# Optimization experiments

Measured on AMD Instinct MI355X. Metric: run time of the kernel, lower is better.

The kernel has to match this reference:

```python
import jax, jax.numpy as jnp
import numpy as np

N, DIM = 4096, 1024

def setup_inputs() -> dict:
    key = jax.random.key(0)
    ks = jax.random.split(key, 5)
    scale = 1.0 / np.sqrt(DIM)
    return {
        "x": jax.random.normal(ks[0], (N, DIM), dtype=jnp.float32),
        "Wq": jax.random.normal(ks[1], (DIM, DIM), dtype=jnp.float32) * scale,
        "bq": jax.random.normal(ks[2], (DIM,), dtype=jnp.float32) * 0.01,
        "Wk": jax.random.normal(ks[3], (DIM, DIM), dtype=jnp.float32) * scale,
        "bk": jax.random.normal(ks[4], (DIM,), dtype=jnp.float32) * 0.01,
    }

def reference(x, Wq, bq, Wk, bk):
    # torch nn.Linear: y = x @ W.T + b
    q = x @ Wq.T + bq            # [N, D]
    k = x @ Wk.T + bk            # [N, D]
    scores = q @ k.T             # [N, N] (no 1/sqrt(d) scaling, as in source)
    attn = jax.nn.softmax(scores, axis=-1)
    return attn @ x              # weighted pooling over raw x (no value proj)
```

## Files before the change

kernel.cpp:

```cpp
#include <hip/hip_runtime.h>
#include <hip/hip_bf16.h>
#include <hip/hip_fp16.h>
#include <stdint.h>


using half8   = __attribute__((ext_vector_type(8))) _Float16;
using float4v = __attribute__((ext_vector_type(4))) float;
using int4v   = __attribute__((ext_vector_type(4))) int;
using uint2v  = __attribute__((ext_vector_type(2))) unsigned int;

#define QS        (6.0f / 32768.0f)
#define INV_S     (32768.0f / 6.0f)
#define INV_S256  (128.0f / 6.0f)
#define C_HH      (65536.0f * QS * QS)
#define C_X       (256.0f * QS * QS)

#define SX        (6.0f / 32768.0f)
#define SW        (0.25f / 32768.0f)
#define P_HH      (65536.0f * SX * SW)
#define P_X       (256.0f * SX * SW)

#define GLOAD_LDS16(gptr, ldsptr)                                              \
  __builtin_amdgcn_global_load_lds(                                            \
      (__attribute__((address_space(1))) void*)(uintptr_t)(gptr),              \
      (__attribute__((address_space(3))) void*)(unsigned)(uintptr_t)(ldsptr),  \
      16, 0, 0)

__device__ __forceinline__ void barrier_raw() {
  asm volatile("" ::: "memory");
  __builtin_amdgcn_s_barrier();
  asm volatile("" ::: "memory");
}

__device__ __forceinline__ int swz3(int row) {
  return (((row >> 2) & 3) << 1) ^ (row & 3);
}

__global__ __launch_bounds__(256, 2) void gemm_s_stats(
    const int8_t* __restrict__ Ahi, const int8_t* __restrict__ Alo,
    const int8_t* __restrict__ Bhi, const int8_t* __restrict__ Blo,
    _Float16* __restrict__ E, float2* __restrict__ stats)
{
  __shared__ __align__(16) int8_t smem[65536];
  int8_t* sAh = smem;
  int8_t* sAl = smem + 16384;
  int8_t* sBh = smem + 32768;
  int8_t* sBl = smem + 49152;

  const int tid  = threadIdx.x;
  const int wave = tid >> 6;
  const int lane = tid & 63;
  const int quad = lane >> 4;
  const int t16  = lane & 15;
  const int wm   = wave & 1;
  const int wn   = wave >> 1;
  const int row0 = blockIdx.y * 128;
  const int col0 = blockIdx.x * 128;

  const int seg  = lane & 3;
  const int rsub = lane >> 2;

  const int offA0 = (row0 + wave * 16 + rsub) * 2048 + seg * 16;
  const int offA1 = offA0 + 64 * 2048;
  const int offB0 = (col0 + wave * 16 + rsub) * 2048 + seg * 16;
  const int offB1 = offB0 + 64 * 2048;
  const int ldsT0 = (wave * 16) * 64;
  const int ldsT1 = (64 + wave * 16) * 64;

  int4v hh[4][4], cc[4][4];
#pragma unroll
  for (int i = 0; i < 4; ++i)
#pragma unroll
    for (int j = 0; j < 4; ++j) {
      hh[i][j] = (int4v){0, 0, 0, 0};
      cc[i][j] = (int4v){0, 0, 0, 0};
    }

  auto stage_k = [&](int ks, int b) {
    const int k0 = ks * 64;
    GLOAD_LDS16(Ahi + offA0 + k0, sAh + b * 8192 + ldsT0);
    GLOAD_LDS16(Ahi + offA1 + k0, sAh + b * 8192 + ldsT1);
    GLOAD_LDS16(Alo + offA0 + k0, sAl + b * 8192 + ldsT0);
    GLOAD_LDS16(Alo + offA1 + k0, sAl + b * 8192 + ldsT1);
    GLOAD_LDS16(Bhi + offB0 + k0, sBh + b * 8192 + ldsT0);
    GLOAD_LDS16(Bhi + offB1 + k0, sBh + b * 8192 + ldsT1);
    GLOAD_LDS16(Blo + offB0 + k0, sBl + b * 8192 + ldsT0);
    GLOAD_LDS16(Blo + offB1 + k0, sBl + b * 8192 + ldsT1);
  };

  stage_k(0, 0);
  asm volatile("s_waitcnt vmcnt(0)" ::: "memory");
  barrier_raw();

  int buf = 0;
  for (int ks = 0; ks < 16; ++ks) {
    if (ks < 15) stage_k(ks + 1, buf ^ 1);

    int4v ah[4], al[4], bh[4], bl[4];
#pragma unroll
    for (int i = 0; i < 4; ++i) {
      const int ao = buf * 8192 + (wm * 64 + i * 16 + t16) * 64 + quad * 16;
      ah[i] = *(const int4v*)(sAh + ao);
      al[i] = *(const int4v*)(sAl + ao);
    }
#pragma unroll
    for (int j = 0; j < 4; ++j) {
      const int bo = buf * 8192 + (wn * 64 + j * 16 + t16) * 64 + quad * 16;
      bh[j] = *(const int4v*)(sBh + bo);
      bl[j] = *(const int4v*)(sBl + bo);
    }

    __builtin_amdgcn_s_setprio(1);
#pragma unroll
    for (int i = 0; i < 4; ++i)
#pragma unroll
      for (int j = 0; j < 4; ++j) {
        hh[i][j] = __builtin_amdgcn_mfma_i32_16x16x64_i8(ah[i], bh[j], hh[i][j], 0, 0, 0);
        cc[i][j] = __builtin_amdgcn_mfma_i32_16x16x64_i8(ah[i], bl[j], cc[i][j], 0, 0, 0);
        cc[i][j] = __builtin_amdgcn_mfma_i32_16x16x64_i8(al[i], bh[j], cc[i][j], 0, 0, 0);
      }
    __builtin_amdgcn_s_setprio(0);

    if (ks < 15) asm volatile("s_waitcnt vmcnt(0)" ::: "memory");
    barrier_raw();
    buf ^= 1;
  }

  float* red = (float*)smem;

  float vv[4][4][4];
  float rmax[4][4];
#pragma unroll
  for (int i = 0; i < 4; ++i)
#pragma unroll
    for (int r = 0; r < 4; ++r) {
      float mx = -3.0e38f;
#pragma unroll
      for (int j = 0; j < 4; ++j) {
        float v = C_HH * (float)hh[i][j][r] + C_X * (float)cc[i][j][r];
        vv[i][j][r] = v;
        mx = fmaxf(mx, v);
      }
      mx = fmaxf(mx, __shfl_xor(mx, 1));
      mx = fmaxf(mx, __shfl_xor(mx, 2));
      mx = fmaxf(mx, __shfl_xor(mx, 4));
      mx = fmaxf(mx, __shfl_xor(mx, 8));
      rmax[i][r] = mx;
    }
  if (t16 == 0) {
#pragma unroll
    for (int i = 0; i < 4; ++i)
#pragma unroll
      for (int r = 0; r < 4; ++r)
        red[wn * 128 + wm * 64 + i * 16 + quad * 4 + r] = rmax[i][r];
  }
  __syncthreads();

  float mrow[4][4];
#pragma unroll
  for (int i = 0; i < 4; ++i)
#pragma unroll
    for (int r = 0; r < 4; ++r) {
      const int row = wm * 64 + i * 16 + quad * 4 + r;
      mrow[i][r] = fmaxf(red[row], red[128 + row]);
    }

  float rsum[4][4];
#pragma unroll
  for (int i = 0; i < 4; ++i)
#pragma unroll
    for (int r = 0; r < 4; ++r) {
      float s = 0.f;
#pragma unroll
      for (int j = 0; j < 4; ++j) {
        float e = __expf(vv[i][j][r] - mrow[i][r]);
        vv[i][j][r] = e;
        s += e;
      }
      s += __shfl_xor(s, 1);
      s += __shfl_xor(s, 2);
      s += __shfl_xor(s, 4);
      s += __shfl_xor(s, 8);
      rsum[i][r] = s;
    }
  if (t16 == 0) {
#pragma unroll
    for (int i = 0; i < 4; ++i)
#pragma unroll
      for (int r = 0; r < 4; ++r)
        red[256 + wn * 128 + wm * 64 + i * 16 + quad * 4 + r] = rsum[i][r];
  }

  uint16_t* img = (uint16_t*)(smem + 32768);
#pragma unroll
  for (int i = 0; i < 4; ++i)
#pragma unroll
    for (int j = 0; j < 4; ++j)
#pragma unroll
      for (int r = 0; r < 4; ++r) {
        const int row  = wm * 64 + i * 16 + quad * 4 + r;
        const int col  = wn * 64 + j * 16 + t16;
        const int colS = col ^ (((quad << 1) ^ r) << 3);
        _Float16 h = (_Float16)vv[i][j][r];
        img[row * 128 + colS] = *(const uint16_t*)&h;
      }
  __syncthreads();

#pragma unroll
  for (int it = 0; it < 8; ++it) {
    const int row    = wave * 32 + it * 4 + quad;
    const int chunkS = t16 ^ swz3(row);
    int4v v = *(const int4v*)&img[row * 128 + chunkS * 8];
    *(int4v*)&E[(size_t)(row0 + row) * 4096 + col0 + t16 * 8] = v;
  }

  if (wn == 0 && t16 == 0) {
#pragma unroll
    for (int i = 0; i < 4; ++i)
#pragma unroll
      for (int r = 0; r < 4; ++r) {
        const int row = wm * 64 + i * 16 + quad * 4 + r;
        const float l = red[256 + row] + red[256 + 128 + row];
        stats[(size_t)(row0 + row) * 32 + blockIdx.x] =
            make_float2(mrow[i][r], l);
      }
  }
}

__global__ __launch_bounds__(256, 2) void gemm_proj_i8(
    const int8_t* __restrict__ Ahi, const int8_t* __restrict__ Alo,
    const int8_t* __restrict__ Bhi, const int8_t* __restrict__ Blo,
    const float* __restrict__ biasQ, const float* __restrict__ biasK,
    int8_t* __restrict__ Ch, int8_t* __restrict__ Cl)
{
  __shared__ __align__(16) int8_t smem[65536];
  int8_t* sAh = smem;
  int8_t* sAl = smem + 16384;
  int8_t* sBh = smem + 32768;
  int8_t* sBl = smem + 49152;

  const int tid  = threadIdx.x;
  const int wave = tid >> 6;
  const int lane = tid & 63;
  const int quad = lane >> 4;
  const int t16  = lane & 15;
  const int wm   = wave & 1;
  const int wn   = wave >> 1;
  const int row0 = blockIdx.y * 128;
  const int col0 = blockIdx.x * 128;

  const int seg  = lane & 3;
  const int rsub = lane >> 2;

  const int offA0 = (row0 + wave * 16 + rsub) * 1024 + seg * 16;
  const int offA1 = offA0 + 64 * 1024;
  const int offB0 = (col0 + wave * 16 + rsub) * 1024 + seg * 16;
  const int offB1 = offB0 + 64 * 1024;
  const int ldsT0 = (wave * 16) * 64;
  const int ldsT1 = (64 + wave * 16) * 64;

  int4v hh[4][4], cc[4][4];
#pragma unroll
  for (int i = 0; i < 4; ++i)
#pragma unroll
    for (int j = 0; j < 4; ++j) {
      hh[i][j] = (int4v){0, 0, 0, 0};
      cc[i][j] = (int4v){0, 0, 0, 0};
    }

  auto stage_k = [&](int ks, int b) {
    const int k0 = ks * 64;
    GLOAD_LDS16(Ahi + offA0 + k0, sAh + b * 8192 + ldsT0);
    GLOAD_LDS16(Ahi + offA1 + k0, sAh + b * 8192 + ldsT1);
    GLOAD_LDS16(Alo + offA0 + k0, sAl + b * 8192 + ldsT0);
    GLOAD_LDS16(Alo + offA1 + k0, sAl + b * 8192 + ldsT1);
    GLOAD_LDS16(Bhi + offB0 + k0, sBh + b * 8192 + ldsT0);
    GLOAD_LDS16(Bhi + offB1 + k0, sBh + b * 8192 + ldsT1);
    GLOAD_LDS16(Blo + offB0 + k0, sBl + b * 8192 + ldsT0);
    GLOAD_LDS16(Blo + offB1 + k0, sBl + b * 8192 + ldsT1);
  };

  stage_k(0, 0);
  asm volatile("s_waitcnt vmcnt(0)" ::: "memory");
  barrier_raw();

  int buf = 0;
  for (int ks = 0; ks < 16; ++ks) {
    if (ks < 15) stage_k(ks + 1, buf ^ 1);

    int4v ah[4], al[4], bh[4], bl[4];
#pragma unroll
    for (int i = 0; i < 4; ++i) {
      const int ao = buf * 8192 + (wm * 64 + i * 16 + t16) * 64 + quad * 16;
      ah[i] = *(const int4v*)(sAh + ao);
      al[i] = *(const int4v*)(sAl + ao);
    }
#pragma unroll
    for (int j = 0; j < 4; ++j) {
      const int bo = buf * 8192 + (wn * 64 + j * 16 + t16) * 64 + quad * 16;
      bh[j] = *(const int4v*)(sBh + bo);
      bl[j] = *(const int4v*)(sBl + bo);
    }

    __builtin_amdgcn_s_setprio(1);
#pragma unroll
    for (int i = 0; i < 4; ++i)
#pragma unroll
      for (int j = 0; j < 4; ++j) {
        hh[i][j] = __builtin_amdgcn_mfma_i32_16x16x64_i8(ah[i], bh[j], hh[i][j], 0, 0, 0);
        cc[i][j] = __builtin_amdgcn_mfma_i32_16x16x64_i8(ah[i], bl[j], cc[i][j], 0, 0, 0);
        cc[i][j] = __builtin_amdgcn_mfma_i32_16x16x64_i8(al[i], bh[j], cc[i][j], 0, 0, 0);
      }
    __builtin_amdgcn_s_setprio(0);

    if (ks < 15) asm volatile("s_waitcnt vmcnt(0)" ::: "memory");
    barrier_raw();
    buf ^= 1;
  }

  uint16_t* img = (uint16_t*)(smem + 32768);
#pragma unroll
  for (int i = 0; i < 4; ++i) {
#pragma unroll
    for (int j = 0; j < 4; ++j) {
      const int ccol = col0 + wn * 64 + j * 16 + t16;
      const float* bp = (ccol < 1024) ? biasQ : (biasK - 1024);
#pragma unroll
      for (int r = 0; r < 4; ++r) {
        float v = P_HH * (float)hh[i][j][r] + P_X * (float)cc[i][j][r] + bp[ccol];
        int hi = (int)lrintf(v * INV_S256);
        hi = hi > 127 ? 127 : (hi < -127 ? -127 : hi);
        int lo = (int)lrintf(v * INV_S - 256.0f * (float)hi);
        lo = lo > 127 ? 127 : (lo < -127 ? -127 : lo);
        const int row  = wm * 64 + i * 16 + quad * 4 + r;
        const int col  = wn * 64 + j * 16 + t16;
        const int colS = col ^ (((quad << 1) ^ r) << 3);
        img[row * 128 + colS] = (uint16_t)((hi & 0xff) | ((lo & 0xff) << 8));
      }
    }
  }
  __syncthreads();

#pragma unroll
  for (int it = 0; it < 8; ++it) {
    const int row    = wave * 32 + it * 4 + quad;
    const int chunkS = t16 ^ swz3(row);
    int4v p = *(const int4v*)&img[row * 128 + chunkS * 8];
    const unsigned w0 = (unsigned)p[0], w1 = (unsigned)p[1];
    const unsigned w2 = (unsigned)p[2], w3 = (unsigned)p[3];
    uint2v hw, lw;
    hw[0] = (w0 & 0xffu) | (((w0 >> 16) & 0xffu) << 8) |
            ((w1 & 0xffu) << 16) | (((w1 >> 16) & 0xffu) << 24);
    hw[1] = (w2 & 0xffu) | (((w2 >> 16) & 0xffu) << 8) |
            ((w3 & 0xffu) << 16) | (((w3 >> 16) & 0xffu) << 24);
    lw[0] = ((w0 >> 8) & 0xffu) | (((w0 >> 24) & 0xffu) << 8) |
            (((w1 >> 8) & 0xffu) << 16) | ((w1 >> 24) << 24);
    lw[1] = ((w2 >> 8) & 0xffu) | (((w2 >> 24) & 0xffu) << 8) |
            (((w3 >> 8) & 0xffu) << 16) | ((w3 >> 24) << 24);
    const size_t go = (size_t)(row0 + row) * 2048 + col0 + t16 * 8;
    *(uint2v*)&Ch[go] = hw;
    *(uint2v*)&Cl[go] = lw;
  }
}

__global__ __launch_bounds__(512) void gemm_av(
    const uint16_t* __restrict__ E, const uint16_t* __restrict__ B,
    const float2* __restrict__ stats, float* __restrict__ out)
{
  __shared__ __align__(16) uint16_t stg[2][2][16384];
  __shared__ float betaS[128 * 33];

  const int L      = blockIdx.x;
  const int xcd    = L & 7;
  const int rest   = L >> 3;
  const int colb   = rest & 7;
  const int bandHi = rest >> 3;
  const int band   = xcd + 8 * bandHi;
  const int row0   = band * 128;
  const int col0   = colb * 128;

  const int tid  = threadIdx.x;
  const int wave = tid >> 6;
  const int z    = wave >> 2;
  const int gw   = wave & 3;
  const int lane = tid & 63;
  const int quad = lane >> 4;
  const int t16  = lane & 15;
  const int wm   = gw & 1;
  const int wn   = gw >> 1;

  const int c8   = lane & 7;
  const int r8   = lane >> 3;
  const int srcC = (c8 - r8) & 7;

  int offA[4], offB[4];
#pragma unroll
  for (int r = 0; r < 4; ++r) {
    offA[r] = (row0 + r * 32 + gw * 8 + r8) * 4096 + srcC * 8;
    offB[r] = (col0 + r * 32 + gw * 8 + r8) * 4096 + srcC * 8;
  }

  auto stage_s = [&](int s, int b) {
    const int k0h = (z * 16 + (s >> 1)) * 128 + (s & 1) * 64;
    uint16_t* sA = &stg[b][z][0];
    uint16_t* sB = &stg[b][z][8192];
#pragma unroll
    for (int r = 0; r < 4; ++r) {
      GLOAD_LDS16(E + offA[r] + k0h, &sA[(r * 32 + gw * 8) * 64]);
      GLOAD_LDS16(B + offB[r] + k0h, &sB[(r * 32 + gw * 8) * 64]);
    }
  };

  stage_s(0, 0);

  if (tid < 128) {
    const int row = row0 + tid;
    float2 st[32];
    float m = -3.0e38f;
#pragma unroll
    for (int t = 0; t < 32; ++t) {
      st[t] = stats[(size_t)row * 32 + t];
      m = fmaxf(m, st[t].x);
    }
    float l = 0.f;
#pragma unroll
    for (int t = 0; t < 32; ++t) l += st[t].y * __expf(st[t].x - m);
    const float inv = 1.0f / l;
#pragma unroll
    for (int t = 0; t < 32; ++t)
      betaS[tid * 33 + t] = __expf(st[t].x - m) * inv;
  }
  asm volatile("s_waitcnt vmcnt(0)" ::: "memory");
  __syncthreads();

  float4v acc[4][4];
#pragma unroll
  for (int i = 0; i < 4; ++i)
#pragma unroll
    for (int j = 0; j < 4; ++j)
      acc[i][j] = (float4v){0.f, 0.f, 0.f, 0.f};

  int buf = 0;
  for (int s = 0; s < 32; ++s) {
    if (s < 31) stage_s(s + 1, buf ^ 1);

    const int t = z * 16 + (s >> 1);
    _Float16 bb[4];
#pragma unroll
    for (int i = 0; i < 4; ++i)
      bb[i] = (_Float16)betaS[(wm * 64 + i * 16 + t16) * 33 + t];

    const uint16_t* sA = &stg[buf][z][0];
    const uint16_t* sB = &stg[buf][z][8192];

    half8 af[2][4], bf[2][4];
#pragma unroll
    for (int ks = 0; ks < 2; ++ks) {
#pragma unroll
      for (int i = 0; i < 4; ++i) {
        const int row = wm * 64 + i * 16 + t16;
        const int ch  = (ks * 4 + quad + (t16 & 7)) & 7;
        af[ks][i] = *(const half8*)&sA[row * 64 + ch * 8];
        half8 bs;
#pragma unroll
        for (int c = 0; c < 8; ++c) bs[c] = bb[i];
        af[ks][i] = af[ks][i] * bs;
      }
#pragma unroll
      for (int j = 0; j < 4; ++j) {
        const int row = wn * 64 + j * 16 + t16;
        const int ch  = (ks * 4 + quad + (t16 & 7)) & 7;
        bf[ks][j] = *(const half8*)&sB[row * 64 + ch * 8];
      }
    }

    __builtin_amdgcn_s_setprio(1);
#pragma unroll
    for (int ks = 0; ks < 2; ++ks)
#pragma unroll
      for (int i = 0; i < 4; ++i)
#pragma unroll
        for (int j = 0; j < 4; ++j)
          acc[i][j] = __builtin_amdgcn_mfma_f32_16x16x32_f16(af[ks][i], bf[ks][j], acc[i][j], 0, 0, 0);
    __builtin_amdgcn_s_setprio(0);

    if (s < 31) asm volatile("s_waitcnt vmcnt(0)" ::: "memory");
    barrier_raw();
    buf ^= 1;
  }

  float* xfer = (float*)stg;
#pragma unroll
  for (int h = 0; h < 2; ++h) {
    if (z == 1) {
#pragma unroll
      for (int i = 2 * h; i < 2 * h + 2; ++i)
#pragma unroll
        for (int j = 0; j < 4; ++j)
#pragma unroll
          for (int r = 0; r < 4; ++r) {
            const int e = (i - 2 * h) * 16 + j * 4 + r;
            xfer[e * 256 + gw * 64 + lane] = acc[i][j][r];
          }
    }
    __syncthreads();
    if (z == 0) {
#pragma unroll
      for (int i = 2 * h; i < 2 * h + 2; ++i)
#pragma unroll
        for (int j = 0; j < 4; ++j)
#pragma unroll
          for (int r = 0; r < 4; ++r) {
            const int e = (i - 2 * h) * 16 + j * 4 + r;
            acc[i][j][r] += xfer[e * 256 + gw * 64 + lane];
          }
    }
    __syncthreads();
  }

  float* img = (float*)((int8_t*)stg + 65536);
  if (z == 0) {
#pragma unroll
    for (int i = 0; i < 4; ++i)
#pragma unroll
      for (int j = 0; j < 4; ++j)
#pragma unroll
        for (int r = 0; r < 4; ++r) {
          const int row  = wm * 64 + i * 16 + quad * 4 + r;
          const int col  = wn * 64 + j * 16 + t16;
          const int colS = col ^ (((quad << 1) ^ r) << 2);
          img[row * 128 + colS] = acc[i][j][r];
        }
  }
  __syncthreads();

#pragma unroll
  for (int it = 0; it < 8; ++it) {
    const int row    = wave * 16 + (lane >> 2);
    const int chunk  = (lane & 3) * 8 + it;
    const int chunkS = chunk ^ swz3(row);
    float4v v = *(const float4v*)&img[row * 128 + chunkS * 4];
    *(float4v*)&out[(size_t)(row0 + row) * 1024 + col0 + chunk * 4] = v;
  }
}

__global__ __launch_bounds__(256) void quantT(
    const float* __restrict__ x, const float* __restrict__ Wq,
    const float* __restrict__ Wk,
    int8_t* __restrict__ xhi, int8_t* __restrict__ xlo,
    int8_t* __restrict__ whi, int8_t* __restrict__ wlo,
    uint16_t* __restrict__ xT)
{
  if (blockIdx.x < 6144) {
// ... 37 lines not shown
      const int oc = ty + p * 8;
      __half hv = __float2half_rn(tile[tx][oc]);
      xT[(size_t)(bx * 32 + oc) * 4096 + by * 32 + tx] = *(uint16_t*)&hv;
    }
  }
}

extern "C" void kernel_launch(void* const* d_in, const int* in_sizes, int n_in,
                              void* d_out, int out_size, void* d_ws, size_t ws_size,
                              hipStream_t stream) {
  const int N = 4096, D = 1024;
  const float* x  = (const float*)d_in[0];
  const float* Wq = (const float*)d_in[1];
  const float* bq = (const float*)d_in[2];
  const float* Wk = (const float*)d_in[3];
  const float* bk = (const float*)d_in[4];
  float* out = (float*)d_out;

  char* w = (char*)d_ws;
  const size_t MiB = 1024 * 1024;
  int8_t*    xq_hi  = (int8_t*)   (w + 0  * MiB);
  int8_t*    xq_lo  = (int8_t*)   (w + 4  * MiB);
  int8_t*    Wqk_hi = (int8_t*)   (w + 8  * MiB);
  int8_t*    Wqk_lo = (int8_t*)   (w + 10 * MiB);
  int8_t*    qk_hi  = (int8_t*)   (w + 12 * MiB);
  int8_t*    qk_lo  = (int8_t*)   (w + 20 * MiB);
  _Float16*  E      = (_Float16*) (w + 36 * MiB);
  float2*    stats  = (float2*)   (w + 68 * MiB);
  uint16_t*  xTh    = (uint16_t*) (w + 72 * MiB);

  quantT<<<10240, 256, 0, stream>>>(x, Wq, Wk, xq_hi, xq_lo, Wqk_hi, Wqk_lo,
                                    xTh);

  gemm_proj_i8<<<dim3(2048 / 128, N / 128), 256, 0, stream>>>(
      xq_hi, xq_lo, Wqk_hi, Wqk_lo, bq, bk, qk_hi, qk_lo);

  gemm_s_stats<<<dim3(N / 128, N / 128), 256, 0, stream>>>(
      qk_hi, qk_lo, qk_hi + 1024, qk_lo + 1024, E, stats);

  gemm_av<<<256, 512, 0, stream>>>((const uint16_t*)E, xTh, stats, out);

  (void)in_sizes; (void)n_in; (void)out_size; (void)ws_size;
}
```

Measured before the change: 218.2 us.

## Enlarge GEMM tiles to 256x128 with 512 threads and triple-buffer loads

The int8 projection and score GEMMs now use 256x128 tiles computed by 8 waves, which shares each B tile across more rows. Their shared-memory staging becomes a three-stage ring with partial vmcnt waits, so loads run two k-steps ahead of compute. The attention-times-x kernel also moves to three buffers with a smaller k chunk per stage. The aim is to hide global-load latency and cut B-operand traffic. In exchange each block needs 144KB of LDS, which drops residency to one block per CU and reduces the grid size.

```diff
diff --git a/kernel.cpp b/kernel.cpp
--- a/kernel.cpp
+++ b/kernel.cpp
@@ -36,36 +36,30 @@
   return (((row >> 2) & 3) << 1) ^ (row & 3);
 }
 
-__global__ __launch_bounds__(256, 2) void gemm_s_stats(
+__global__ __launch_bounds__(512, 2) void gemm_s_stats(
     const int8_t* __restrict__ Ahi, const int8_t* __restrict__ Alo,
     const int8_t* __restrict__ Bhi, const int8_t* __restrict__ Blo,
     _Float16* __restrict__ E, float2* __restrict__ stats)
 {
-  __shared__ __align__(16) int8_t smem[65536];
-  int8_t* sAh = smem;
-  int8_t* sAl = smem + 16384;
-  int8_t* sBh = smem + 32768;
-  int8_t* sBl = smem + 49152;
+  __shared__ __align__(16) int8_t smem[147456];
 
   const int tid  = threadIdx.x;
   const int wave = tid >> 6;
   const int lane = tid & 63;
   const int quad = lane >> 4;
   const int t16  = lane & 15;
-  const int wm   = wave & 1;
-  const int wn   = wave >> 1;
-  const int row0 = blockIdx.y * 128;
+  const int wm   = wave >> 1;
+  const int wn   = wave & 1;
+  const int row0 = blockIdx.y * 256;
   const int col0 = blockIdx.x * 128;
 
   const int seg  = lane & 3;
-  const int rsub = lane >> 2;
-
-  const int offA0 = (row0 + wave * 16 + rsub) * 2048 + seg * 16;
-  const int offA1 = offA0 + 64 * 2048;
-  const int offB0 = (col0 + wave * 16 + rsub) * 2048 + seg * 16;
-  const int offB1 = offB0 + 64 * 2048;
-  const int ldsT0 = (wave * 16) * 64;
-  const int ldsT1 = (64 + wave * 16) * 64;
+  const int arow = wave * 16 + (lane >> 2);
+
+  const int gA0 = (row0 + arow) * 2048 + seg * 16;
+  const int gA1 = gA0 + 128 * 2048;
+  const int gB0 = (col0 + arow) * 2048 + seg * 16;
+  const int ldsW = wave * 1024;
 
   int4v hh[4][4], cc[4][4];
 #pragma unroll
@@ -78,36 +72,36 @@
 
   auto stage_k = [&](int ks, int b) {
     const int k0 = ks * 64;
-    GLOAD_LDS16(Ahi + offA0 + k0, sAh + b * 8192 + ldsT0);
-    GLOAD_LDS16(Ahi + offA1 + k0, sAh + b * 8192 + ldsT1);
-    GLOAD_LDS16(Alo + offA0 + k0, sAl + b * 8192 + ldsT0);
-    GLOAD_LDS16(Alo + offA1 + k0, sAl + b * 8192 + ldsT1);
-    GLOAD_LDS16(Bhi + offB0 + k0, sBh + b * 8192 + ldsT0);
-    GLOAD_LDS16(Bhi + offB1 + k0, sBh + b * 8192 + ldsT1);
-    GLOAD_LDS16(Blo + offB0 + k0, sBl + b * 8192 + ldsT0);
-    GLOAD_LDS16(Blo + offB1 + k0, sBl + b * 8192 + ldsT1);
+    int8_t* base = smem + b * 49152;
+    GLOAD_LDS16(Ahi + gA0 + k0, base + ldsW);
+    GLOAD_LDS16(Ahi + gA1 + k0, base + 8192 + ldsW);
+    GLOAD_LDS16(Alo + gA0 + k0, base + 16384 + ldsW);
+    GLOAD_LDS16(Alo + gA1 + k0, base + 16384 + 8192 + ldsW);
+    GLOAD_LDS16(Bhi + gB0 + k0, base + 32768 + ldsW);
+    GLOAD_LDS16(Blo + gB0 + k0, base + 40960 + ldsW);
   };
 
   stage_k(0, 0);
-  asm volatile("s_waitcnt vmcnt(0)" ::: "memory");
+  stage_k(1, 1);
+  asm volatile("s_waitcnt vmcnt(6)" ::: "memory");
   barrier_raw();
 
-  int buf = 0;
   for (int ks = 0; ks < 16; ++ks) {
-    if (ks < 15) stage_k(ks + 1, buf ^ 1);
+    int8_t* base = smem + (ks % 3) * 49152;
+    if (ks < 14) stage_k(ks + 2, (ks + 2) % 3);
 
     int4v ah[4], al[4], bh[4], bl[4];
 #pragma unroll
     for (int i = 0; i < 4; ++i) {
-      const int ao = buf * 8192 + (wm * 64 + i * 16 + t16) * 64 + quad * 16;
-      ah[i] = *(const int4v*)(sAh + ao);
-      al[i] = *(const int4v*)(sAl + ao);
+      const int ao = (wm * 64 + i * 16 + t16) * 64 + quad * 16;
+      ah[i] = *(const int4v*)(base + ao);
+      al[i] = *(const int4v*)(base + 16384 + ao);
     }
 #pragma unroll
     for (int j = 0; j < 4; ++j) {
-      const int bo = buf * 8192 + (wn * 64 + j * 16 + t16) * 64 + quad * 16;
-      bh[j] = *(const int4v*)(sBh + bo);
-      bl[j] = *(const int4v*)(sBl + bo);
+      const int bo = (wn * 64 + j * 16 + t16) * 64 + quad * 16;
+      bh[j] = *(const int4v*)(base + 32768 + bo);
+      bl[j] = *(const int4v*)(base + 40960 + bo);
     }
 
     __builtin_amdgcn_s_setprio(1);
@@ -121,12 +115,15 @@
       }
     __builtin_amdgcn_s_setprio(0);
 
-    if (ks < 15) asm volatile("s_waitcnt vmcnt(0)" ::: "memory");
-    barrier_raw();
-    buf ^= 1;
-  }
-
-  float* red = (float*)smem;
+    if (ks < 15) {
+      if (ks < 14) asm volatile("s_waitcnt vmcnt(6)" ::: "memory");
+      else         asm volatile("s_waitcnt vmcnt(0)" ::: "memory");
+      barrier_raw();
+    }
+  }
+  barrier_raw();
+
+  float* red = (float*)(smem + 65536);
 
   float vv[4][4][4];
   float rmax[4][4];
@@ -152,7 +149,7 @@
     for (int i = 0; i < 4; ++i)
 #pragma unroll
       for (int r = 0; r < 4; ++r)
-        red[wn * 128 + wm * 64 + i * 16 + quad * 4 + r] = rmax[i][r];
+        red[wn * 256 + wm * 64 + i * 16 + quad * 4 + r] = rmax[i][r];
   }
   __syncthreads();
 
@@ -162,7 +159,7 @@
 #pragma unroll
     for (int r = 0; r < 4; ++r) {
       const int row = wm * 64 + i * 16 + quad * 4 + r;
-      mrow[i][r] = fmaxf(red[row], red[128 + row]);
+      mrow[i][r] = fmaxf(red[row], red[256 + row]);
     }
 
   float rsum[4][4];
@@ -188,10 +185,10 @@
     for (int i = 0; i < 4; ++i)
 #pragma unroll
       for (int r = 0; r < 4; ++r)
-        red[256 + wn * 128 + wm * 64 + i * 16 + quad * 4 + r] = rsum[i][r];
-  }
-
-  uint16_t* img = (uint16_t*)(smem + 32768);
+        red[512 + wn * 256 + wm * 64 + i * 16 + quad * 4 + r] = rsum[i][r];
+  }
+
+  uint16_t* img = (uint16_t*)smem;
 #pragma unroll
   for (int i = 0; i < 4; ++i)
 #pragma unroll
@@ -200,7 +197,7 @@
       for (int r = 0; r < 4; ++r) {
         const int row  = wm * 64 + i * 16 + quad * 4 + r;
         const int col  = wn * 64 + j * 16 + t16;
-        const int colS = col ^ (((quad << 1) ^ r) << 3);
+        const int colS = col ^ (swz3(row) << 3);
         _Float16 h = (_Float16)vv[i][j][r];
         img[row * 128 + colS] = *(const uint16_t*)&h;
       }
@@ -214,50 +211,38 @@
     *(int4v*)&E[(size_t)(row0 + row) * 4096 + col0 + t16 * 8] = v;
   }
 
-  if (wn == 0 && t16 == 0) {
-#pragma unroll
-    for (int i = 0; i < 4; ++i)
-#pragma unroll
-      for (int r = 0; r < 4; ++r) {
-        const int row = wm * 64 + i * 16 + quad * 4 + r;
-        const float l = red[256 + row] + red[256 + 128 + row];
-        stats[(size_t)(row0 + row) * 32 + blockIdx.x] =
-            make_float2(mrow[i][r], l);
-      }
+  if (tid < 256) {
+    const float m = fmaxf(red[tid], red[256 + tid]);
+    const float l = red[512 + tid] + red[768 + tid];
+    stats[(size_t)(row0 + tid) * 32 + blockIdx.x] = make_float2(m, l);
   }
 }
 
-__global__ __launch_bounds__(256, 2) void gemm_proj_i8(
+__global__ __launch_bounds__(512, 2) void gemm_proj_i8(
     const int8_t* __restrict__ Ahi, const int8_t* __restrict__ Alo,
     const int8_t* __restrict__ Bhi, const int8_t* __restrict__ Blo,
     const float* __restrict__ biasQ, const float* __restrict__ biasK,
     int8_t* __restrict__ Ch, int8_t* __restrict__ Cl)
 {
-  __shared__ __align__(16) int8_t smem[65536];
-  int8_t* sAh = smem;
-  int8_t* sAl = smem + 16384;
-  int8_t* sBh = smem + 32768;
-  int8_t* sBl = smem + 49152;
+  __shared__ __align__(16) int8_t smem[147456];
 
   const int tid  = threadIdx.x;
   const int wave = tid >> 6;
   const int lane = tid & 63;
   const int quad = lane >> 4;
   const int t16  = lane & 15;
-  const int wm   = wave & 1;
-  const int wn   = wave >> 1;
-  const int row0 = blockIdx.y * 128;
+  const int wm   = wave >> 1;
+  const int wn   = wave & 1;
+  const int row0 = blockIdx.y * 256;
   const int col0 = blockIdx.x * 128;
 
   const int seg  = lane & 3;
-  const int rsub = lane >> 2;
-
-  const int offA0 = (row0 + wave * 16 + rsub) * 1024 + seg * 16;
-  const int offA1 = offA0 + 64 * 1024;
-  const int offB0 = (col0 + wave * 16 + rsub) * 1024 + seg * 16;
-  const int offB1 = offB0 + 64 * 1024;
-  const int ldsT0 = (wave * 16) * 64;
-  const int ldsT1 = (64 + wave * 16) * 64;
+  const int arow = wave * 16 + (lane >> 2);
+
+  const int gA0 = (row0 + arow) * 1024 + seg * 16;
+  const int gA1 = gA0 + 128 * 1024;
+  const int gB0 = (col0 + arow) * 1024 + seg * 16;
+  const int ldsW = wave * 1024;
 
   int4v hh[4][4], cc[4][4];
 #pragma unroll
@@ -270,36 +255,36 @@
 
   auto stage_k = [&](int ks, int b) {
     const int k0 = ks * 64;
-    GLOAD_LDS16(Ahi + offA0 + k0, sAh + b * 8192 + ldsT0);
-    GLOAD_LDS16(Ahi + offA1 + k0, sAh + b * 8192 + ldsT1);
-    GLOAD_LDS16(Alo + offA0 + k0, sAl + b * 8192 + ldsT0);
-    GLOAD_LDS16(Alo + offA1 + k0, sAl + b * 8192 + ldsT1);
-    GLOAD_LDS16(Bhi + offB0 + k0, sBh + b * 8192 + ldsT0);
-    GLOAD_LDS16(Bhi + offB1 + k0, sBh + b * 8192 + ldsT1);
-    GLOAD_LDS16(Blo + offB0 + k0, sBl + b * 8192 + ldsT0);
-    GLOAD_LDS16(Blo + offB1 + k0, sBl + b * 8192 + ldsT1);
+    int8_t* base = smem + b * 49152;
+    GLOAD_LDS16(Ahi + gA0 + k0, base + ldsW);
+    GLOAD_LDS16(Ahi + gA1 + k0, base + 8192 + ldsW);
+    GLOAD_LDS16(Alo + gA0 + k0, base + 16384 + ldsW);
+    GLOAD_LDS16(Alo + gA1 + k0, base + 16384 + 8192 + ldsW);
+    GLOAD_LDS16(Bhi + gB0 + k0, base + 32768 + ldsW);
+    GLOAD_LDS16(Blo + gB0 + k0, base + 40960 + ldsW);
   };
 
   stage_k(0, 0);
-  asm volatile("s_waitcnt vmcnt(0)" ::: "memory");
+  stage_k(1, 1);
+  asm volatile("s_waitcnt vmcnt(6)" ::: "memory");
   barrier_raw();
 
-  int buf = 0;
   for (int ks = 0; ks < 16; ++ks) {
-    if (ks < 15) stage_k(ks + 1, buf ^ 1);
+    int8_t* base = smem + (ks % 3) * 49152;
+    if (ks < 14) stage_k(ks + 2, (ks + 2) % 3);
 
     int4v ah[4], al[4], bh[4], bl[4];
 #pragma unroll
     for (int i = 0; i < 4; ++i) {
-      const int ao = buf * 8192 + (wm * 64 + i * 16 + t16) * 64 + quad * 16;
-      ah[i] = *(const int4v*)(sAh + ao);
-      al[i] = *(const int4v*)(sAl + ao);
+      const int ao = (wm * 64 + i * 16 + t16) * 64 + quad * 16;
+      ah[i] = *(const int4v*)(base + ao);
+      al[i] = *(const int4v*)(base + 16384 + ao);
     }
 #pragma unroll
     for (int j = 0; j < 4; ++j) {
-      const int bo = buf * 8192 + (wn * 64 + j * 16 + t16) * 64 + quad * 16;
-      bh[j] = *(const int4v*)(sBh + bo);
-      bl[j] = *(const int4v*)(sBl + bo);
+      const int bo = (wn * 64 + j * 16 + t16) * 64 + quad * 16;
+      bh[j] = *(const int4v*)(base + 32768 + bo);
+      bl[j] = *(const int4v*)(base + 40960 + bo);
     }
 
     __builtin_amdgcn_s_setprio(1);
@@ -313,12 +298,15 @@
       }
     __builtin_amdgcn_s_setprio(0);
 
-    if (ks < 15) asm volatile("s_waitcnt vmcnt(0)" ::: "memory");
-    barrier_raw();
-    buf ^= 1;
-  }
-
-  uint16_t* img = (uint16_t*)(smem + 32768);
+    if (ks < 15) {
+      if (ks < 14) asm volatile("s_waitcnt vmcnt(6)" ::: "memory");
+      else         asm volatile("s_waitcnt vmcnt(0)" ::: "memory");
+      barrier_raw();
+    }
+  }
+  barrier_raw();
+
+  uint16_t* img = (uint16_t*)smem;
 #pragma unroll
   for (int i = 0; i < 4; ++i) {
 #pragma unroll
@@ -334,7 +322,7 @@
         lo = lo > 127 ? 127 : (lo < -127 ? -127 : lo);
         const int row  = wm * 64 + i * 16 + quad * 4 + r;
         const int col  = wn * 64 + j * 16 + t16;
-        const int colS = col ^ (((quad << 1) ^ r) << 3);
+        const int colS = col ^ (swz3(row) << 3);
         img[row * 128 + colS] = (uint16_t)((hi & 0xff) | ((lo & 0xff) << 8));
       }
     }
@@ -367,7 +355,7 @@
     const uint16_t* __restrict__ E, const uint16_t* __restrict__ B,
     const float2* __restrict__ stats, float* __restrict__ out)
 {
-  __shared__ __align__(16) uint16_t stg[2][2][16384];
+  __shared__ __align__(16) uint16_t stg[3][16384];
   __shared__ float betaS[128 * 33];
 
   const int L      = blockIdx.x;
@@ -389,29 +377,26 @@
   const int wm   = gw & 1;
   const int wn   = gw >> 1;
 
-  const int c8   = lane & 7;
-  const int r8   = lane >> 3;
-  const int srcC = (c8 - r8) & 7;
-
-  int offA[4], offB[4];
-#pragma unroll
-  for (int r = 0; r < 4; ++r) {
-    offA[r] = (row0 + r * 32 + gw * 8 + r8) * 4096 + srcC * 8;
-    offB[r] = (col0 + r * 32 + gw * 8 + r8) * 4096 + srcC * 8;
-  }
+  const int seg  = lane & 3;
+  const int grow = gw * 16 + (lane >> 2);
+
+  const int offA0 = (row0 + grow) * 4096 + seg * 8;
+  const int offA1 = offA0 + 64 * 4096;
+  const int offB0 = (col0 + grow) * 4096 + seg * 8;
+  const int offB1 = offB0 + 64 * 4096;
+  const int ldsW  = gw * 512;
 
   auto stage_s = [&](int s, int b) {
-    const int k0h = (z * 16 + (s >> 1)) * 128 + (s & 1) * 64;
-    uint16_t* sA = &stg[b][z][0];
-    uint16_t* sB = &stg[b][z][8192];
-#pragma unroll
-    for (int r = 0; r < 4; ++r) {
-      GLOAD_LDS16(E + offA[r] + k0h, &sA[(r * 32 + gw * 8) * 64]);
-      GLOAD_LDS16(B + offB[r] + k0h, &sB[(r * 32 + gw * 8) * 64]);
-    }
+    const int k0h = (z * 16 + (s >> 2)) * 128 + (s & 3) * 32;
+    uint16_t* dst = &stg[b][z * 8192];
+    GLOAD_LDS16(E + offA0 + k0h, dst + ldsW);
+    GLOAD_LDS16(E + offA1 + k0h, dst + 2048 + ldsW);
+    GLOAD_LDS16(B + offB0 + k0h, dst + 4096 + ldsW);
+    GLOAD_LDS16(B + offB1 + k0h, dst + 4096 + 2048 + ldsW);
   };
 
   stage_s(0, 0);
+  stage_s(1, 1);
 
   if (tid < 128) {
     const int row = row0 + tid;
@@ -430,7 +415,7 @@
     for (int t = 0; t < 32; ++t)
       betaS[tid * 33 + t] = __expf(st[t].x - m) * inv;
   }
-  asm volatile("s_waitcnt vmcnt(0)" ::: "memory");
+  asm volatile("s_waitcnt vmcnt(4)" ::: "memory");
   __syncthreads();
 
   float4v acc[4][4];
@@ -440,54 +425,44 @@
     for (int j = 0; j < 4; ++j)
       acc[i][j] = (float4v){0.f, 0.f, 0.f, 0.f};
 
-  int buf = 0;
-  for (int s = 0; s < 32; ++s) {
-    if (s < 31) stage_s(s + 1, buf ^ 1);
-
-    const int t = z * 16 + (s >> 1);
+  for (int s = 0; s < 64; ++s) {
+    const uint16_t* base = &stg[s % 3][z * 8192];
+    if (s < 62) stage_s(s + 2, (s + 2) % 3);
+
+    const int t = z * 16 + (s >> 2);
     _Float16 bb[4];
 #pragma unroll
     for (int i = 0; i < 4; ++i)
       bb[i] = (_Float16)betaS[(wm * 64 + i * 16 + t16) * 33 + t];
 
-    const uint16_t* sA = &stg[buf][z][0];
-    const uint16_t* sB = &stg[buf][z][8192];
-
-    half8 af[2][4], bf[2][4];
-#pragma unroll
-    for (int ks = 0; ks < 2; ++ks) {
-#pragma unroll
-      for (int i = 0; i < 4; ++i) {
-        const int row = wm * 64 + i * 16 + t16;
-        const int ch  = (ks * 4 + quad + (t16 & 7)) & 7;
-        af[ks][i] = *(const half8*)&sA[row * 64 + ch * 8];
-        half8 bs;
-#pragma unroll
-        for (int c = 0; c < 8; ++c) bs[c] = bb[i];
-        af[ks][i] = af[ks][i] * bs;
-      }
-#pragma unroll
-      for (int j = 0; j < 4; ++j) {
-        const int row = wn * 64 + j * 16 + t16;
-        const int ch  = (ks * 4 + quad + (t16 & 7)) & 7;
-        bf[ks][j] = *(const half8*)&sB[row * 64 + ch * 8];
-      }
-    }
+    half8 af[4], bf[4];
+#pragma unroll
+    for (int i = 0; i < 4; ++i) {
+      af[i] = *(const half8*)&base[(wm * 64 + i * 16 + t16) * 32 + quad * 8];
+      half8 bs;
+#pragma unroll
+      for (int c = 0; c < 8; ++c) bs[c] = bb[i];
+      af[i] = af[i] * bs;
+    }
+#pragma unroll
+    for (int j = 0; j < 4; ++j)
+      bf[j] = *(const half8*)&base[4096 + (wn * 64 + j * 16 + t16) * 32 + quad * 8];
 
     __builtin_amdgcn_s_setprio(1);
 #pragma unroll
-    for (int ks = 0; ks < 2; ++ks)
-#pragma unroll
-      for (int i = 0; i < 4; ++i)
-#pragma unroll
-        for (int j = 0; j < 4; ++j)
-          acc[i][j] = __builtin_amdgcn_mfma_f32_16x16x32_f16(af[ks][i], bf[ks][j], acc[i][j], 0, 0, 0);
+    for (int i = 0; i < 4; ++i)
+#pragma unroll
+      for (int j = 0; j < 4; ++j)
+        acc[i][j] = __builtin_amdgcn_mfma_f32_16x16x32_f16(af[i], bf[j], acc[i][j], 0, 0, 0);
     __builtin_amdgcn_s_setprio(0);
 
-    if (s < 31) asm volatile("s_waitcnt vmcnt(0)" ::: "memory");
-    barrier_raw();
-    buf ^= 1;
-  }
+    if (s < 63) {
+      if (s < 62) asm volatile("s_waitcnt vmcnt(4)" ::: "memory");
+      else        asm volatile("s_waitcnt vmcnt(0)" ::: "memory");
+      barrier_raw();
+    }
+  }
+  barrier_raw();
 
   float* xfer = (float*)stg;
 #pragma unroll
@@ -518,7 +493,7 @@
     __syncthreads();
   }
 
-  float* img = (float*)((int8_t*)stg + 65536);
+  float* img = (float*)stg;
   if (z == 0) {
 #pragma unroll
     for (int i = 0; i < 4; ++i)
@@ -622,10 +597,10 @@
   quantT<<<10240, 256, 0, stream>>>(x, Wq, Wk, xq_hi, xq_lo, Wqk_hi, Wqk_lo,
                                     xTh);
 
-  gemm_proj_i8<<<dim3(2048 / 128, N / 128), 256, 0, stream>>>(
+  gemm_proj_i8<<<dim3(2048 / 128, N / 256), 512, 0, stream>>>(
       xq_hi, xq_lo, Wqk_hi, Wqk_lo, bq, bk, qk_hi, qk_lo);
 
-  gemm_s_stats<<<dim3(N / 128, N / 128), 256, 0, stream>>>(
+  gemm_s_stats<<<dim3(N / 128, N / 256), 512, 0, stream>>>(
       qk_hi, qk_lo, qk_hi + 1024, qk_lo + 1024, E, stats);
 
   gemm_av<<<256, 512, 0, stream>>>((const uint16_t*)E, xTh, stats, out);
```

New measurement: 223.5 us. +2.4%, slower.

## Load E fragments directly to registers and halve LDS staging in gemm_av

Applied to the files above, without the earlier changes.

In gemm_av, the E (probability) operand is now read straight from global memory into register fragments, double-buffered across steps. Only B goes through LDS, which halves the LDS staging buffer and changes the B swizzle to XOR. This should lower LDS traffic and footprint, which may allow more occupancy. The trade-offs are more registers, uncoalesced-ish global reads for E, and the img region now aliasing the xfer area. The int8 GEMMs also reorder their LDS loads and MFMA issue into three separate passes, which may improve instruction interleaving.

```diff
diff --git a/kernel.cpp b/kernel.cpp
--- a/kernel.cpp
+++ b/kernel.cpp
@@ -101,12 +101,20 @@
     for (int i = 0; i < 4; ++i) {
       const int ao = buf * 8192 + (wm * 64 + i * 16 + t16) * 64 + quad * 16;
       ah[i] = *(const int4v*)(sAh + ao);
-      al[i] = *(const int4v*)(sAl + ao);
     }
 #pragma unroll
     for (int j = 0; j < 4; ++j) {
       const int bo = buf * 8192 + (wn * 64 + j * 16 + t16) * 64 + quad * 16;
       bh[j] = *(const int4v*)(sBh + bo);
+    }
+#pragma unroll
+    for (int i = 0; i < 4; ++i) {
+      const int ao = buf * 8192 + (wm * 64 + i * 16 + t16) * 64 + quad * 16;
+      al[i] = *(const int4v*)(sAl + ao);
+    }
+#pragma unroll
+    for (int j = 0; j < 4; ++j) {
+      const int bo = buf * 8192 + (wn * 64 + j * 16 + t16) * 64 + quad * 16;
       bl[j] = *(const int4v*)(sBl + bo);
     }
 
@@ -114,11 +122,18 @@
 #pragma unroll
     for (int i = 0; i < 4; ++i)
 #pragma unroll
-      for (int j = 0; j < 4; ++j) {
+      for (int j = 0; j < 4; ++j)
         hh[i][j] = __builtin_amdgcn_mfma_i32_16x16x64_i8(ah[i], bh[j], hh[i][j], 0, 0, 0);
+#pragma unroll
+    for (int i = 0; i < 4; ++i)
+#pragma unroll
+      for (int j = 0; j < 4; ++j)
         cc[i][j] = __builtin_amdgcn_mfma_i32_16x16x64_i8(ah[i], bl[j], cc[i][j], 0, 0, 0);
+#pragma unroll
+    for (int i = 0; i < 4; ++i)
+#pragma unroll
+      for (int j = 0; j < 4; ++j)
         cc[i][j] = __builtin_amdgcn_mfma_i32_16x16x64_i8(al[i], bh[j], cc[i][j], 0, 0, 0);
-      }
     __builtin_amdgcn_s_setprio(0);
 
     if (ks < 15) asm volatile("s_waitcnt vmcnt(0)" ::: "memory");
@@ -293,12 +308,20 @@
     for (int i = 0; i < 4; ++i) {
       const int ao = buf * 8192 + (wm * 64 + i * 16 + t16) * 64 + quad * 16;
       ah[i] = *(const int4v*)(sAh + ao);
-      al[i] = *(const int4v*)(sAl + ao);
     }
 #pragma unroll
     for (int j = 0; j < 4; ++j) {
       const int bo = buf * 8192 + (wn * 64 + j * 16 + t16) * 64 + quad * 16;
       bh[j] = *(const int4v*)(sBh + bo);
+    }
+#pragma unroll
+    for (int i = 0; i < 4; ++i) {
+      const int ao = buf * 8192 + (wm * 64 + i * 16 + t16) * 64 + quad * 16;
+      al[i] = *(const int4v*)(sAl + ao);
+    }
+#pragma unroll
+    for (int j = 0; j < 4; ++j) {
+      const int bo = buf * 8192 + (wn * 64 + j * 16 + t16) * 64 + quad * 16;
       bl[j] = *(const int4v*)(sBl + bo);
     }
 
@@ -306,11 +329,18 @@
 #pragma unroll
     for (int i = 0; i < 4; ++i)
 #pragma unroll
-      for (int j = 0; j < 4; ++j) {
+      for (int j = 0; j < 4; ++j)
         hh[i][j] = __builtin_amdgcn_mfma_i32_16x16x64_i8(ah[i], bh[j], hh[i][j], 0, 0, 0);
+#pragma unroll
+    for (int i = 0; i < 4; ++i)
+#pragma unroll
+      for (int j = 0; j < 4; ++j)
         cc[i][j] = __builtin_amdgcn_mfma_i32_16x16x64_i8(ah[i], bl[j], cc[i][j], 0, 0, 0);
+#pragma unroll
+    for (int i = 0; i < 4; ++i)
+#pragma unroll
+      for (int j = 0; j < 4; ++j)
         cc[i][j] = __builtin_amdgcn_mfma_i32_16x16x64_i8(al[i], bh[j], cc[i][j], 0, 0, 0);
-      }
     __builtin_amdgcn_s_setprio(0);
 
     if (ks < 15) asm volatile("s_waitcnt vmcnt(0)" ::: "memory");
@@ -367,7 +397,7 @@
     const uint16_t* __restrict__ E, const uint16_t* __restrict__ B,
     const float2* __restrict__ stats, float* __restrict__ out)
 {
-  __shared__ __align__(16) uint16_t stg[2][2][16384];
+  __shared__ __align__(16) uint16_t stg[2][2][8192];
   __shared__ float betaS[128 * 33];
 
   const int L      = blockIdx.x;
@@ -389,29 +419,42 @@
   const int wm   = gw & 1;
   const int wn   = gw >> 1;
 
-  const int c8   = lane & 7;
-  const int r8   = lane >> 3;
-  const int srcC = (c8 - r8) & 7;
-
-  int offA[4], offB[4];
-#pragma unroll
-  for (int r = 0; r < 4; ++r) {
-    offA[r] = (row0 + r * 32 + gw * 8 + r8) * 4096 + srcC * 8;
-    offB[r] = (col0 + r * 32 + gw * 8 + r8) * 4096 + srcC * 8;
-  }
-
-  auto stage_s = [&](int s, int b) {
-    const int k0h = (z * 16 + (s >> 1)) * 128 + (s & 1) * 64;
-    uint16_t* sA = &stg[b][z][0];
-    uint16_t* sB = &stg[b][z][8192];
-#pragma unroll
-    for (int r = 0; r < 4; ++r) {
-      GLOAD_LDS16(E + offA[r] + k0h, &sA[(r * 32 + gw * 8) * 64]);
-      GLOAD_LDS16(B + offB[r] + k0h, &sB[(r * 32 + gw * 8) * 64]);
-    }
+  const int r8 = lane >> 3;
+  const int c8 = lane & 7;
+
+  int offE[2][4];
+#pragma unroll
+  for (int ks = 0; ks < 2; ++ks)
+#pragma unroll
+    for (int i = 0; i < 4; ++i)
+      offE[ks][i] = (row0 + wm * 64 + i * 16 + t16) * 4096 + z * 2048 +
+                    ks * 32 + quad * 8;
+
+  int offB[4];
+#pragma unroll
+  for (int p = 0; p < 4; ++p)
+    offB[p] = (col0 + p * 32 + gw * 8 + r8) * 8192 + z * 4096 + ((c8 ^ r8) * 16);
+
+  auto stage_B = [&](int s, int b) {
+    const int k0b = s * 128;
+    int8_t* dst = (int8_t*)&stg[b][z][0];
+#pragma unroll
+    for (int p = 0; p < 4; ++p)
+      GLOAD_LDS16((const int8_t*)B + offB[p] + k0b, dst + (p * 32 + gw * 8) * 128);
   };
 
-  stage_s(0, 0);
+  half8 afA[2][4], afB[2][4];
+  auto load_E = [&](int s, half8 (&dstf)[2][4]) {
+    const int k0h = s * 64;
+#pragma unroll
+    for (int ks = 0; ks < 2; ++ks)
+#pragma unroll
+      for (int i = 0; i < 4; ++i)
+        dstf[ks][i] = *(const half8*)&E[offE[ks][i] + k0h];
+  };
+
+  stage_B(0, 0);
+  load_E(0, afA);
 
   if (tid < 128) {
     const int row = row0 + tid;
@@ -440,9 +483,11 @@
     for (int j = 0; j < 4; ++j)
       acc[i][j] = (float4v){0.f, 0.f, 0.f, 0.f};
 
-  int buf = 0;
-  for (int s = 0; s < 32; ++s) {
-    if (s < 31) stage_s(s + 1, buf ^ 1);
+  auto step = [&](int s, int b, half8 (&cur)[2][4], half8 (&nxt)[2][4]) {
+    if (s < 31) {
+      load_E(s + 1, nxt);
+      stage_B(s + 1, b ^ 1);
+    }
 
     const int t = z * 16 + (s >> 1);
     _Float16 bb[4];
@@ -450,43 +495,43 @@
     for (int i = 0; i < 4; ++i)
       bb[i] = (_Float16)betaS[(wm * 64 + i * 16 + t16) * 33 + t];
 
-    const uint16_t* sA = &stg[buf][z][0];
-    const uint16_t* sB = &stg[buf][z][8192];
-
-    half8 af[2][4], bf[2][4];
-#pragma unroll
-    for (int ks = 0; ks < 2; ++ks) {
-#pragma unroll
-      for (int i = 0; i < 4; ++i) {
-        const int row = wm * 64 + i * 16 + t16;
-        const int ch  = (ks * 4 + quad + (t16 & 7)) & 7;
-        af[ks][i] = *(const half8*)&sA[row * 64 + ch * 8];
-        half8 bs;
-#pragma unroll
-        for (int c = 0; c < 8; ++c) bs[c] = bb[i];
-        af[ks][i] = af[ks][i] * bs;
-      }
+    const uint16_t* sB = &stg[b][z][0];
+    half8 bf[2][4];
+#pragma unroll
+    for (int ks = 0; ks < 2; ++ks)
 #pragma unroll
       for (int j = 0; j < 4; ++j) {
         const int row = wn * 64 + j * 16 + t16;
-        const int ch  = (ks * 4 + quad + (t16 & 7)) & 7;
+        const int ch  = (ks * 4 + quad) ^ (t16 & 7);
         bf[ks][j] = *(const half8*)&sB[row * 64 + ch * 8];
       }
-    }
 
     __builtin_amdgcn_s_setprio(1);
 #pragma unroll
-    for (int ks = 0; ks < 2; ++ks)
+    for (int ks = 0; ks < 2; ++ks) {
+      half8 afs[4];
+#pragma unroll
+      for (int i = 0; i < 4; ++i) {
+        half8 bs;
+#pragma unroll
+        for (int c = 0; c < 8; ++c) bs[c] = bb[i];
+        afs[i] = cur[ks][i] * bs;
+      }
 #pragma unroll
       for (int i = 0; i < 4; ++i)
 #pragma unroll
         for (int j = 0; j < 4; ++j)
-          acc[i][j] = __builtin_amdgcn_mfma_f32_16x16x32_f16(af[ks][i], bf[ks][j], acc[i][j], 0, 0, 0);
+          acc[i][j] = __builtin_amdgcn_mfma_f32_16x16x32_f16(afs[i], bf[ks][j], acc[i][j], 0, 0, 0);
+    }
     __builtin_amdgcn_s_setprio(0);
 
     if (s < 31) asm volatile("s_waitcnt vmcnt(0)" ::: "memory");
     barrier_raw();
-    buf ^= 1;
+  };
+
+  for (int s2 = 0; s2 < 32; s2 += 2) {
+    step(s2,     0, afA, afB);
+    step(s2 + 1, 1, afB, afA);
   }
 
   float* xfer = (float*)stg;
@@ -518,7 +563,7 @@
     __syncthreads();
   }
 
-  float* img = (float*)((int8_t*)stg + 65536);
+  float* img = (float*)stg;
   if (z == 0) {
 #pragma unroll
     for (int i = 0; i < 4; ++i)
```

New measurement: 266.7 us. 22.2% more time.

## Split int8 hi/lo operand staging into three waves with partial vmcnt waits

Applied to the files above, without the earlier changes.

Splits each K-step's global-to-LDS staging into three groups (Ahi+Bhi, Blo, Alo). Each group is issued right before the MFMA phase that uses it, gated by partial s_waitcnt vmcnt counts and a barrier. The goal is to start MFMAs on the hi-hi product before the lo tiles arrive, so global load latency overlaps with compute instead of waiting for all 8 loads each step. In exchange there are three barriers per K-step instead of one, and correctness depends on the vmcnt counts matching the number of loads still outstanding.

```diff
diff --git a/kernel.cpp b/kernel.cpp
--- a/kernel.cpp
+++ b/kernel.cpp
@@ -76,53 +76,90 @@
       cc[i][j] = (int4v){0, 0, 0, 0};
     }
 
-  auto stage_k = [&](int ks, int b) {
+  auto stage_AhBh = [&](int ks, int b) {
     const int k0 = ks * 64;
     GLOAD_LDS16(Ahi + offA0 + k0, sAh + b * 8192 + ldsT0);
     GLOAD_LDS16(Ahi + offA1 + k0, sAh + b * 8192 + ldsT1);
-    GLOAD_LDS16(Alo + offA0 + k0, sAl + b * 8192 + ldsT0);
-    GLOAD_LDS16(Alo + offA1 + k0, sAl + b * 8192 + ldsT1);
     GLOAD_LDS16(Bhi + offB0 + k0, sBh + b * 8192 + ldsT0);
     GLOAD_LDS16(Bhi + offB1 + k0, sBh + b * 8192 + ldsT1);
+  };
+  auto stage_Bl = [&](int ks, int b) {
+    const int k0 = ks * 64;
     GLOAD_LDS16(Blo + offB0 + k0, sBl + b * 8192 + ldsT0);
     GLOAD_LDS16(Blo + offB1 + k0, sBl + b * 8192 + ldsT1);
   };
-
-  stage_k(0, 0);
-  asm volatile("s_waitcnt vmcnt(0)" ::: "memory");
-  barrier_raw();
+  auto stage_Al = [&](int ks, int b) {
+    const int k0 = ks * 64;
+    GLOAD_LDS16(Alo + offA0 + k0, sAl + b * 8192 + ldsT0);
+    GLOAD_LDS16(Alo + offA1 + k0, sAl + b * 8192 + ldsT1);
+  };
+
+  stage_AhBh(0, 0);
+  stage_Bl(0, 0);
+  stage_Al(0, 0);
 
   int buf = 0;
   for (int ks = 0; ks < 16; ++ks) {
-    if (ks < 15) stage_k(ks + 1, buf ^ 1);
-
-    int4v ah[4], al[4], bh[4], bl[4];
-#pragma unroll
-    for (int i = 0; i < 4; ++i) {
-      const int ao = buf * 8192 + (wm * 64 + i * 16 + t16) * 64 + quad * 16;
-      ah[i] = *(const int4v*)(sAh + ao);
-      al[i] = *(const int4v*)(sAl + ao);
-    }
-#pragma unroll
-    for (int j = 0; j < 4; ++j) {
-      const int bo = buf * 8192 + (wn * 64 + j * 16 + t16) * 64 + quad * 16;
-      bh[j] = *(const int4v*)(sBh + bo);
-      bl[j] = *(const int4v*)(sBl + bo);
-    }
+    asm volatile("s_waitcnt vmcnt(4)" ::: "memory");
+    barrier_raw();
+    if (ks < 15) stage_AhBh(ks + 1, buf ^ 1);
+
+    int4v ah[4], bh[4];
+#pragma unroll
+    for (int i = 0; i < 4; ++i)
+      ah[i] = *(const int4v*)(sAh + buf * 8192 +
+                              (wm * 64 + i * 16 + t16) * 64 + quad * 16);
+#pragma unroll
+    for (int j = 0; j < 4; ++j)
+      bh[j] = *(const int4v*)(sBh + buf * 8192 +
+                              (wn * 64 + j * 16 + t16) * 64 + quad * 16);
 
     __builtin_amdgcn_s_setprio(1);
 #pragma unroll
     for (int i = 0; i < 4; ++i)
 #pragma unroll
-      for (int j = 0; j < 4; ++j) {
+      for (int j = 0; j < 4; ++j)
         hh[i][j] = __builtin_amdgcn_mfma_i32_16x16x64_i8(ah[i], bh[j], hh[i][j], 0, 0, 0);
+    __builtin_amdgcn_s_setprio(0);
+
+    if (ks < 15) asm volatile("s_waitcnt vmcnt(6)" ::: "memory");
+    else         asm volatile("s_waitcnt vmcnt(2)" ::: "memory");
+    barrier_raw();
+    if (ks < 15) stage_Bl(ks + 1, buf ^ 1);
+
+    int4v bl[4];
+#pragma unroll
+    for (int j = 0; j < 4; ++j)
+      bl[j] = *(const int4v*)(sBl + buf * 8192 +
+                              (wn * 64 + j * 16 + t16) * 64 + quad * 16);
+
+    __builtin_amdgcn_s_setprio(1);
+#pragma unroll
+    for (int i = 0; i < 4; ++i)
+#pragma unroll
+      for (int j = 0; j < 4; ++j)
         cc[i][j] = __builtin_amdgcn_mfma_i32_16x16x64_i8(ah[i], bl[j], cc[i][j], 0, 0, 0);
+    __builtin_amdgcn_s_setprio(0);
+
+    if (ks < 15) asm volatile("s_waitcnt vmcnt(6)" ::: "memory");
+    else         asm volatile("s_waitcnt vmcnt(0)" ::: "memory");
+    barrier_raw();
+    if (ks < 15) stage_Al(ks + 1, buf ^ 1);
+
+    int4v al[4];
+#pragma unroll
+    for (int i = 0; i < 4; ++i)
+      al[i] = *(const int4v*)(sAl + buf * 8192 +
+                              (wm * 64 + i * 16 + t16) * 64 + quad * 16);
+
+    __builtin_amdgcn_s_setprio(1);
+#pragma unroll
+    for (int i = 0; i < 4; ++i)
+#pragma unroll
+      for (int j = 0; j < 4; ++j)
         cc[i][j] = __builtin_amdgcn_mfma_i32_16x16x64_i8(al[i], bh[j], cc[i][j], 0, 0, 0);
-      }
     __builtin_amdgcn_s_setprio(0);
 
-    if (ks < 15) asm volatile("s_waitcnt vmcnt(0)" ::: "memory");
-    barrier_raw();
     buf ^= 1;
   }
 
@@ -268,53 +305,90 @@
       cc[i][j] = (int4v){0, 0, 0, 0};
     }
 
-  auto stage_k = [&](int ks, int b) {
+  auto stage_AhBh = [&](int ks, int b) {
     const int k0 = ks * 64;
     GLOAD_LDS16(Ahi + offA0 + k0, sAh + b * 8192 + ldsT0);
     GLOAD_LDS16(Ahi + offA1 + k0, sAh + b * 8192 + ldsT1);
-    GLOAD_LDS16(Alo + offA0 + k0, sAl + b * 8192 + ldsT0);
-    GLOAD_LDS16(Alo + offA1 + k0, sAl + b * 8192 + ldsT1);
     GLOAD_LDS16(Bhi + offB0 + k0, sBh + b * 8192 + ldsT0);
     GLOAD_LDS16(Bhi + offB1 + k0, sBh + b * 8192 + ldsT1);
+  };
+  auto stage_Bl = [&](int ks, int b) {
+    const int k0 = ks * 64;
     GLOAD_LDS16(Blo + offB0 + k0, sBl + b * 8192 + ldsT0);
     GLOAD_LDS16(Blo + offB1 + k0, sBl + b * 8192 + ldsT1);
   };
-
-  stage_k(0, 0);
-  asm volatile("s_waitcnt vmcnt(0)" ::: "memory");
-  barrier_raw();
+  auto stage_Al = [&](int ks, int b) {
+    const int k0 = ks * 64;
+    GLOAD_LDS16(Alo + offA0 + k0, sAl + b * 8192 + ldsT0);
+    GLOAD_LDS16(Alo + offA1 + k0, sAl + b * 8192 + ldsT1);
+  };
+
+  stage_AhBh(0, 0);
+  stage_Bl(0, 0);
+  stage_Al(0, 0);
 
   int buf = 0;
   for (int ks = 0; ks < 16; ++ks) {
-    if (ks < 15) stage_k(ks + 1, buf ^ 1);
-
-    int4v ah[4], al[4], bh[4], bl[4];
-#pragma unroll
-    for (int i = 0; i < 4; ++i) {
-      const int ao = buf * 8192 + (wm * 64 + i * 16 + t16) * 64 + quad * 16;
-      ah[i] = *(const int4v*)(sAh + ao);
-      al[i] = *(const int4v*)(sAl + ao);
-    }
-#pragma unroll
-    for (int j = 0; j < 4; ++j) {
-      const int bo = buf * 8192 + (wn * 64 + j * 16 + t16) * 64 + quad * 16;
-      bh[j] = *(const int4v*)(sBh + bo);
-      bl[j] = *(const int4v*)(sBl + bo);
-    }
+    asm volatile("s_waitcnt vmcnt(4)" ::: "memory");
+    barrier_raw();
+    if (ks < 15) stage_AhBh(ks + 1, buf ^ 1);
+
+    int4v ah[4], bh[4];
+#pragma unroll
+    for (int i = 0; i < 4; ++i)
+      ah[i] = *(const int4v*)(sAh + buf * 8192 +
+                              (wm * 64 + i * 16 + t16) * 64 + quad * 16);
+#pragma unroll
+    for (int j = 0; j < 4; ++j)
+      bh[j] = *(const int4v*)(sBh + buf * 8192 +
+                              (wn * 64 + j * 16 + t16) * 64 + quad * 16);
 
     __builtin_amdgcn_s_setprio(1);
 #pragma unroll
     for (int i = 0; i < 4; ++i)
 #pragma unroll
-      for (int j = 0; j < 4; ++j) {
+      for (int j = 0; j < 4; ++j)
         hh[i][j] = __builtin_amdgcn_mfma_i32_16x16x64_i8(ah[i], bh[j], hh[i][j], 0, 0, 0);
+    __builtin_amdgcn_s_setprio(0);
+
+    if (ks < 15) asm volatile("s_waitcnt vmcnt(6)" ::: "memory");
+    else         asm volatile("s_waitcnt vmcnt(2)" ::: "memory");
+    barrier_raw();
+    if (ks < 15) stage_Bl(ks + 1, buf ^ 1);
+
+    int4v bl[4];
+#pragma unroll
+    for (int j = 0; j < 4; ++j)
+      bl[j] = *(const int4v*)(sBl + buf * 8192 +
+                              (wn * 64 + j * 16 + t16) * 64 + quad * 16);
+
+    __builtin_amdgcn_s_setprio(1);
+#pragma unroll
+    for (int i = 0; i < 4; ++i)
+#pragma unroll
+      for (int j = 0; j < 4; ++j)
         cc[i][j] = __builtin_amdgcn_mfma_i32_16x16x64_i8(ah[i], bl[j], cc[i][j], 0, 0, 0);
+    __builtin_amdgcn_s_setprio(0);
+
+    if (ks < 15) asm volatile("s_waitcnt vmcnt(6)" ::: "memory");
+    else         asm volatile("s_waitcnt vmcnt(0)" ::: "memory");
+    barrier_raw();
+    if (ks < 15) stage_Al(ks + 1, buf ^ 1);
+
+    int4v al[4];
+#pragma unroll
+    for (int i = 0; i < 4; ++i)
+      al[i] = *(const int4v*)(sAl + buf * 8192 +
+                              (wm * 64 + i * 16 + t16) * 64 + quad * 16);
+
+    __builtin_amdgcn_s_setprio(1);
+#pragma unroll
+    for (int i = 0; i < 4; ++i)
+#pragma unroll
+      for (int j = 0; j < 4; ++j)
         cc[i][j] = __builtin_amdgcn_mfma_i32_16x16x64_i8(al[i], bh[j], cc[i][j], 0, 0, 0);
-      }
     __builtin_amdgcn_s_setprio(0);
 
-    if (ks < 15) asm volatile("s_waitcnt vmcnt(0)" ::: "memory");
-    barrier_raw();
     buf ^= 1;
   }
 
```

Result: no change. 215.2 us (-1.4%).
